# Performance work log

Hardware: AMD Instinct MI355X
Metric: run time of the kernel (lower is better)

The kernel has to match this reference:

```python
import jax, jax.numpy as jnp
import numpy as np

WIN_SIZE = 256           # GlobalConfig.win_size (assumed)
NFFT = 2 * WIN_SIZE      # 512 -> NFREQ = 257 rfft bins
HOP = WIN_SIZE
NFREQ = WIN_SIZE + 1
K = 3                    # all kernel sizes in the model
EPS = 1e-5


def _stft(x):
    # x: (B, S) -> (B, T, F, 2) real view of complex STFT (hann window, no center)
    B, S = x.shape
    T = (S - NFFT) // HOP + 1
    n = jnp.arange(NFFT)
    win = 0.5 - 0.5 * jnp.cos(2.0 * jnp.pi * n / NFFT)
    idx = jnp.arange(T)[:, None] * HOP + n[None, :]
    frames = x[:, idx] * win                       # (B, T, NFFT)
    spec = jnp.fft.rfft(frames, axis=-1)           # (B, T, F) complex
    return jnp.stack([spec.real, spec.imag], axis=-1).astype(x.dtype)


def _td_layer(x, W, b, same):
    # time-distributed conv over the frequency axis. x: (B,T,F,Cin), W: (k,Cin,Cout)
    k = W.shape[0]
    if same:
        x = jnp.pad(x, ((0, 0), (0, 0), (k // 2, k - 1 - k // 2), (0, 0)))
    Fout = x.shape[2] - k + 1
    xs = jnp.stack([x[:, :, i:i + Fout] for i in range(k)], axis=0)  # (k,B,T,Fout,Cin)
    return jnp.einsum('kbtfc,kco->btfo', xs, W) + b


def _td_block(x, W1, b1, W2, b2):
    h = jax.nn.relu(_td_layer(x, W1, b1, True))
    return _td_layer(h, W2, b2, True)


def _layer(x, g, beta, dw, W1, b1, W2, b2):
    # LayerNorm over (F, C), causal depthwise conv over T, TD pointwise block, ReLU
    B, T, F, C = x.shape
    mu = x.mean(axis=(-2, -1), keepdims=True)
    var = x.var(axis=(-2, -1), keepdims=True)
    xn = (x - mu) * jax.lax.rsqrt(var + EPS) * g + beta
    h = xn.reshape(B, T, F * C)
    hp = jnp.pad(h, ((0, 0), (K - 1, 0), (0, 0)))   # causal left-pad on time
    y = sum(hp[:, i:i + T, :] * dw[:, i] for i in range(K))  # (B,T,F*C) depthwise
    y = y.reshape(B, T, F, C)
    return jax.nn.relu(_td_block(y, W1, b1, W2, b2))


def setup_inputs() -> dict:
    key = jax.random.key(0)
    ks = iter(jax.random.split(key, 40))
    def rn(shape, s=0.05):
        return (jax.random.normal(next(ks), shape) * s).astype(jnp.float32)
    F = NFREQ
    d = {}
    d['x'] = jax.random.normal(next(ks), (8, 262144), dtype=jnp.float32)
    d['l0_W1'] = rn((3, 2, 4)); d['l0_b1'] = jnp.zeros((4,), jnp.float32)
    d['l0_W2'] = rn((3, 4, 8)); d['l0_b2'] = jnp.zeros((8,), jnp.float32)
    for name, cin in (('l1', 8), ('l2', 16), ('l3', 24)):
        d[name + '_g'] = jnp.ones((F, cin), jnp.float32)
        d[name + '_bn'] = jnp.zeros((F, cin), jnp.float32)
        d[name + '_dw'] = rn((F * cin, 3), 0.3)
        d[name + '_W1'] = rn((3, cin, 8)); d[name + '_b1'] = jnp.zeros((8,), jnp.float32)
        d[name + '_W2'] = rn((3, 8, 8)); d[name + '_b2'] = jnp.zeros((8,), jnp.float32)
    d['fc1_W'] = rn((3, 32, 1)); d['fc1_b'] = jnp.zeros((1,), jnp.float32)
    d['fc2_W'] = rn((F - 2, 1)); d['fc2_b'] = jnp.zeros((1,), jnp.float32)
    return d


def reference(x, l0_W1, l0_b1, l0_W2, l0_b2,
              l1_g, l1_bn, l1_dw, l1_W1, l1_b1, l1_W2, l1_b2,
              l2_g, l2_bn, l2_dw, l2_W1, l2_b1, l2_W2, l2_b2,
              l3_g, l3_bn, l3_dw, l3_W1, l3_b1, l3_W2, l3_b2,
              fc1_W, fc1_b, fc2_W, fc2_b):
    s = _stft(x)                                            # (B,T,F,2)
    h = jax.nn.relu(_td_block(s, l0_W1, l0_b1, l0_W2, l0_b2))  # (B,T,F,8)
    h = jnp.concatenate([h, _layer(h, l1_g, l1_bn, l1_dw, l1_W1, l1_b1, l1_W2, l1_b2)], axis=3)
    h = jnp.concatenate([h, _layer(h, l2_g, l2_bn, l2_dw, l2_W1, l2_b1, l2_W2, l2_b2)], axis=3)
    h = jnp.concatenate([h, _layer(h, l3_g, l3_bn, l3_dw, l3_W1, l3_b1, l3_W2, l3_b2)], axis=3)
    h = jax.nn.relu(_td_layer(h, fc1_W, fc1_b, False))[..., 0]  # (B,T,F-2)
    out = jax.nn.sigmoid(h @ fc2_W + fc2_b)                 # (B,T,1)
    return out[..., 0]                                      # (B,T)
```

## Files before the change

kernel.cpp:

```cpp
#include <hip/hip_runtime.h>
#include <hip/hip_fp16.h>

namespace {

constexpr int BATCH = 8;
constexpr int SLEN  = 262144;
constexpr int TT    = 1023;
constexpr int NF    = 257;
constexpr int NCH   = 24;
constexpr int NBT   = BATCH * TT;
constexpr int FRS   = NCH * NF;
constexpr float EPS = 1e-5f;

typedef _Float16 h2v __attribute__((ext_vector_type(2)));

__device__ inline float fdot2(unsigned a, unsigned b, float c) {
#if __has_builtin(__builtin_amdgcn_fdot2)
  return __builtin_amdgcn_fdot2(__builtin_bit_cast(h2v, a),
                                __builtin_bit_cast(h2v, b), c, false);
#else
  h2v av = __builtin_bit_cast(h2v, a), bv = __builtin_bit_cast(h2v, b);
  return fmaf((float)av[0], (float)bv[0], fmaf((float)av[1], (float)bv[1], c));
#endif
}
__device__ inline unsigned packh2(float a, float b) {
  h2v v; v[0] = (_Float16)a; v[1] = (_Float16)b;
  return __builtin_bit_cast(unsigned, v);
}
__device__ inline unsigned short f2h(float v) {
  return __builtin_bit_cast(unsigned short, (_Float16)v);
}
__device__ inline int div257(int e) { return (e * 65282) >> 24; }

__global__ __launch_bounds__(256, 8) void stft_l0_kernel(
    const float* __restrict__ x,
    const float* __restrict__ W1g, const float* __restrict__ b1g,
    const float* __restrict__ W2g, const float* __restrict__ b2g,
    __half* __restrict__ H, float* __restrict__ stats0)
{
  __shared__ float  xw[512];
  __shared__ __align__(16) float2 abE[128];
  __shared__ __align__(16) float2 abO[128];
  __shared__ float2 oxc[128];
  __shared__ float  sre[NF + 2];
  __shared__ float  sim[NF + 2];
  __shared__ float  h1[4][NF + 2];
  __shared__ float  wW1[24], wb1[4], wW2[96], wb2[8];
  __shared__ float  red[8];

  const int tid = threadIdx.x;
  const int bt  = blockIdx.x;
  const int b   = bt / TT;
  const int t   = bt - b * TT;
  const float* xp = x + (size_t)b * SLEN + (size_t)t * 256;

  if (tid < 24) wW1[tid] = W1g[tid];
  if (tid < 4)  wb1[tid] = b1g[tid];
  if (tid < 96) wW2[tid] = W2g[tid];
  if (tid < 8)  wb2[tid] = b2g[tid];

  const float STEP = 6.283185307179586f / 512.0f;
  for (int n = tid; n < 512; n += 256) {
    float sv, cv;
    sincosf(STEP * (float)n, &sv, &cv);
    xw[n] = xp[n] * (0.5f - 0.5f * cv);
  }
  __syncthreads();

  if (tid < 128) {
    const int n = 2 * tid;
    abE[tid] = (n == 0) ? make_float2(0.f, 0.f)
                        : make_float2(xw[n] + xw[512 - n], xw[n] - xw[512 - n]);
  } else {
    const int n = 2 * (tid - 128) + 1;
    abO[tid - 128] = make_float2(xw[n] + xw[512 - n], xw[n] - xw[512 - n]);
  }
  __syncthreads();

  const float x0 = xw[0], x256 = xw[256];
  {
    const int  k = tid & 127;
    const bool P = (tid >= 128);
    float s1, c1;
    sincosf(STEP * (float)k, &s1, &c1);
    const float c2 = fmaf(c1,c1,-s1*s1), s2 = 2.f*c1*s1;
    const float c3 = fmaf(c2,c1,-s2*s1), s3 = fmaf(c2,s1, s2*c1);
    const float c4 = fmaf(c2,c2,-s2*s2), s4 = 2.f*c2*s2;
    const float c5 = fmaf(c4,c1,-s4*s1), s5 = fmaf(c4,s1, s4*c1);
    const float c6 = fmaf(c4,c2,-s4*s2), s6 = fmaf(c4,s2, s4*c2);
    const float c7 = fmaf(c4,c3,-s4*s3), s7 = fmaf(c4,s3, s4*c3);
    const float c8 = fmaf(c4,c4,-s4*s4), s8 = 2.f*c4*s4;
    float cA = P ? c1 : 1.f, sA = P ? s1 : 0.f;
    float cB = P ? c3 : c2,  sB = P ? s3 : s2;
    float cC = P ? c5 : c4,  sC = P ? s5 : s4;
    float cD = P ? c7 : c6,  sD = P ? s7 : s6;
    const float4* ab4 = P ? (const float4*)abO : (const float4*)abE;
    float re = 0.f, im = 0.f;
    for (int m = 0; m < 32; ++m) {
      const float4 q0 = ab4[2*m];
      const float4 q1 = ab4[2*m + 1];
      re = fmaf(q0.x, cA, re); im = fmaf(q0.y, sA, im);
      re = fmaf(q0.z, cB, re); im = fmaf(q0.w, sB, im);
      re = fmaf(q1.x, cC, re); im = fmaf(q1.y, sC, im);
      re = fmaf(q1.z, cD, re); im = fmaf(q1.w, sD, im);
      float t0;
      t0 = fmaf(cA, c8, -sA*s8); sA = fmaf(cA, s8, sA*c8); cA = t0;
      t0 = fmaf(cB, c8, -sB*s8); sB = fmaf(cB, s8, sB*c8); cB = t0;
      t0 = fmaf(cC, c8, -sC*s8); sC = fmaf(cC, s8, sC*c8); cC = t0;
      t0 = fmaf(cD, c8, -sD*s8); sD = fmaf(cD, s8, sD*c8); cD = t0;
    }
    if (P) oxc[k] = make_float2(re, im);

    float tr = 0.f, ti = 0.f;
    if (tid & 1) {
      const float v = abO[tid >> 1].y;
      ti = ((tid >> 1) & 1) ? v : -v;
    } else {
      const float v = abE[tid >> 1].x;
      tr = ((tid >> 1) & 1) ? -v : v;
    }
    #pragma unroll
    for (int off = 32; off > 0; off >>= 1) {
      tr += __shfl_down(tr, off, 64);
      ti += __shfl_down(ti, off, 64);
    }
    if ((tid & 63) == 0) { red[(tid >> 6)*2] = tr; red[(tid >> 6)*2 + 1] = ti; }
    __syncthreads();

    if (!P) {
      const float rb  = x0 + ((k & 1) ? -x256 : x256);
      const float reo = oxc[k].x, imo = oxc[k].y;
      sre[1 + k]       = rb + re + reo;
      sim[1 + k]       = -(im + imo);
      sre[1 + 256 - k] = rb + re - reo;
      sim[1 + 256 - k] = im - imo;
    }
    if (tid == 0) {
      sre[1 + 128] = x0 + x256 + red[0] + red[2] + red[4] + red[6];
      sim[1 + 128] = red[1] + red[3] + red[5] + red[7];
      sre[0] = 0.f; sim[0] = 0.f; sre[258] = 0.f; sim[258] = 0.f;
    }
  }
  __syncthreads();

  for (int f = tid; f < NF; f += 256) {
    float acc[4] = {wb1[0], wb1[1], wb1[2], wb1[3]};
    #pragma unroll
    for (int i = 0; i < 3; ++i) {
      float vr = sre[f + i], vi = sim[f + i];
      #pragma unroll
      for (int c = 0; c < 4; ++c)
        acc[c] = fmaf(vr, wW1[(i*2+0)*4 + c], fmaf(vi, wW1[(i*2+1)*4 + c], acc[c]));
    }
    #pragma unroll
    for (int c = 0; c < 4; ++c) h1[c][f + 1] = fmaxf(acc[c], 0.f);
  }
  if (tid < 4) { h1[tid][0] = 0.f; h1[tid][NF + 1] = 0.f; }
  __syncthreads();

  const size_t obase = (size_t)bt * FRS;
  float ps1 = 0.f, ps2 = 0.f;
  for (int f = tid; f < NF; f += 256) {
    float acc[8];
    #pragma unroll
    for (int c = 0; c < 8; ++c) acc[c] = wb2[c];
    #pragma unroll
    for (int i = 0; i < 3; ++i)
      #pragma unroll
      for (int c4 = 0; c4 < 4; ++c4) {
        float hv = h1[c4][f + i];
        #pragma unroll
        for (int c = 0; c < 8; ++c)
          acc[c] = fmaf(hv, wW2[(i*4+c4)*8 + c], acc[c]);
      }
    #pragma unroll
    for (int c = 0; c < 8; ++c) {
      const __half hv = __float2half(fmaxf(acc[c], 0.f));
      H[obase + (size_t)c * NF + f] = hv;
      const float v = __half2float(hv);
      ps1 += v;
      ps2 = fmaf(v, v, ps2);
    }
  }
  #pragma unroll
  for (int off = 32; off > 0; off >>= 1) {
    ps1 += __shfl_down(ps1, off, 64);
    ps2 += __shfl_down(ps2, off, 64);
  }
  __syncthreads();
  if ((tid & 63) == 0) { red[(tid >> 6) * 2] = ps1; red[(tid >> 6) * 2 + 1] = ps2; }
  __syncthreads();
  if (tid == 0) {
    stats0[bt * 2]     = red[0] + red[2] + red[4] + red[6];
    stats0[bt * 2 + 1] = red[1] + red[3] + red[5] + red[7];
  }
}

__device__ inline void fold_one(int idx, int CIN,
    const float* g, const float* bn, const float* dw, __half* dst, int NEL) {
  const int c = div257(idx), f = idx - c * 257;
  const int s = f * CIN + c;
  const float gv = g[s], bv = bn[s];
  const float d0 = dw[s*3], d1 = dw[s*3+1], d2 = dw[s*3+2];
  dst[idx]         = __float2half(gv * d0);
  dst[NEL + idx]   = __float2half(gv * d1);
  dst[2*NEL + idx] = __float2half(gv * d2);
  dst[3*NEL + idx] = __float2half(bv * (d0 + d1 + d2));
  dst[4*NEL + idx] = __float2half(bv * (d1 + d2));
  dst[5*NEL + idx] = __float2half(bv * d2);
}

__global__ __launch_bounds__(256) void fold_all(
    const float* g1, const float* bn1, const float* dw1, __half* t1,
    const float* g2, const float* bn2, const float* dw2, __half* t2,
    const float* g3, const float* bn3, const float* dw3, __half* t3)
{
  int idx = blockIdx.x * 256 + threadIdx.x;
  if (idx < 8*257) { fold_one(idx, 8, g1, bn1, dw1, t1, 8*257); return; }
  idx -= 8*257;
  if (idx < 16*257) { fold_one(idx, 16, g2, bn2, dw2, t2, 16*257); return; }
  idx -= 16*257;
  if (idx < 24*257) fold_one(idx, 24, g3, bn3, dw3, t3, 24*257);
}

template<int CIN, bool HEAD>
__global__ __launch_bounds__(256, 8) void layer_bt(
    const __half* __restrict__ H, __half* __restrict__ Hout,
    const float* __restrict__ st0, const float* __restrict__ st1,
    const float* __restrict__ st2, float* __restrict__ stats_out,
    const __half* __restrict__ tbl,
    const float* __restrict__ W1g, const float* __restrict__ b1g,
    const float* __restrict__ W2g, const float* __restrict__ b2g,
    const float* __restrict__ fc1W, const float* __restrict__ fc1b,
    const float* __restrict__ fc2W, const float* __restrict__ fc2b,
    float* __restrict__ out)
{
  constexpr int NEL   = CIN * NF;
  constexpr int NP2   = NEL / 2;
  constexpr int NPER2 = (NP2 + 255) / 256;
  constexpr int TAIL2 = NP2 - 256 * (NPER2 - 1);
  constexpr int PC1   = CIN + 2;
  constexpr int PC2   = 10;
  constexpr int NQ1   = CIN / 2;

  __shared__ unsigned short y_t[259 * PC1];
  __shared__ unsigned short h1_t[259 * PC2];
  __shared__ unsigned w1p[3 * NQ1 * 8];
  __shared__ unsigned w2p[96];
  __shared__ float wb1[8], wb2[8];
  __shared__ float red[8];
  __shared__ unsigned wfc1p[HEAD ? 48 : 1];

  const int tid = threadIdx.x;
  const int bt  = blockIdx.x;
  const int b   = bt / TT;
  const int t   = bt - b * TT;

  for (int idx = tid; idx < 3 * NQ1 * 8; idx += 256) {
    const int o = idx & 7, q = (idx >> 3) % NQ1, i = idx / (NQ1 * 8);
    w1p[idx] = packh2(W1g[(i*CIN + 2*q)*8 + o], W1g[(i*CIN + 2*q + 1)*8 + o]);
  }
  if (tid < 96) {
    const int o = tid & 7, q = (tid >> 3) & 3, i = tid >> 5;
    w2p[tid] = packh2(W2g[(i*8 + 2*q)*8 + o], W2g[(i*8 + 2*q + 1)*8 + o]);
  }
  if (tid < 8) { wb1[tid] = b1g[tid]; wb2[tid] = b2g[tid]; }
  if (tid < PC1) { y_t[tid] = 0; y_t[258*PC1 + tid] = 0; }
  if (tid < PC2) { h1_t[tid] = 0; h1_t[258*PC2 + tid] = 0; }
  if constexpr (HEAD) {
    if (tid < 48) {
      const int q = tid & 15, i = tid >> 4;
      wfc1p[tid] = packh2(fc1W[i*32 + 2*q], fc1W[i*32 + 2*q + 1]);
    }
  }

  float mu0 = 0.f, rs0 = 0.f, mu1 = 0.f, rs1 = 0.f, mu2, rs2;
  {
    const float inv = 1.0f / (float)NEL;
    float s1 = st0[bt*2], s2v = st0[bt*2+1];
    if constexpr (CIN >= 16) { s1 += st1[bt*2]; s2v += st1[bt*2+1]; }
    if constexpr (CIN >= 24) { s1 += st2[bt*2]; s2v += st2[bt*2+1]; }
    mu2 = s1 * inv; rs2 = rsqrtf(s2v * inv - mu2*mu2 + EPS);
    if (t >= 1) {
      const int fb = bt - 1;
      float a = st0[fb*2], c = st0[fb*2+1];
      if constexpr (CIN >= 16) { a += st1[fb*2]; c += st1[fb*2+1]; }
      if constexpr (CIN >= 24) { a += st2[fb*2]; c += st2[fb*2+1]; }
      mu1 = a * inv; rs1 = rsqrtf(c * inv - mu1*mu1 + EPS);
    }
    if (t >= 2) {
      const int fb = bt - 2;
      float a = st0[fb*2], c = st0[fb*2+1];
      if constexpr (CIN >= 16) { a += st1[fb*2]; c += st1[fb*2+1]; }
      if constexpr (CIN >= 24) { a += st2[fb*2]; c += st2[fb*2+1]; }
      mu0 = a * inv; rs0 = rsqrtf(c * inv - mu0*mu0 + EPS);
    }
  }

  const int base = b * TT;
  const __half2* f2p = (const __half2*)(H + (size_t)bt * FRS);
  const __half2* f1p = (const __half2*)(H + (size_t)max(bt - 1, base) * FRS);
  const __half2* f0p = (const __half2*)(H + (size_t)max(bt - 2, base) * FRS);
  const __half2* P0p = (const __half2*)tbl;
  const __half2* P1p = (const __half2*)(tbl + NEL);
  const __half2* P2p = (const __half2*)(tbl + 2 * NEL);
  const int qsel = (t >= 2) ? 0 : (t == 1 ? 1 : 2);
  const __half2* Qp  = (const __half2*)(tbl + (3 + qsel) * NEL);

  #pragma unroll
  for (int j = 0; j < NPER2; ++j) {
    const bool act = (j < NPER2 - 1) || (tid < TAIL2);
    if (act) {
      const int p  = tid + 256 * j;
      const int e0 = 2 * p;
      const int c0 = div257(e0);
      const int fi = e0 - c0 * 257;
      const float2 xa = __half22float2(f0p[p]);
      const float2 xb = __half22float2(f1p[p]);
      const float2 xc = __half22float2(f2p[p]);
      const float2 pa = __half22float2(P0p[p]);
      const float2 pb = __half22float2(P1p[p]);
      const float2 pc = __half22float2(P2p[p]);
      const float2 qq = __half22float2(Qp[p]);
      const float y0 = fmaf((xa.x - mu0) * rs0, pa.x,
                       fmaf((xb.x - mu1) * rs1, pb.x,
                       fmaf((xc.x - mu2) * rs2, pc.x, qq.x)));
      const float y1 = fmaf((xa.y - mu0) * rs0, pa.y,
                       fmaf((xb.y - mu1) * rs1, pb.y,
                       fmaf((xc.y - mu2) * rs2, pc.y, qq.y)));
      const int a1 = (fi + 1) * PC1 + c0;
      y_t[a1] = f2h(y0);
      const int a2 = (fi == 256) ? (PC1 + c0 + 1) : (a1 + PC1);
      y_t[a2] = f2h(y1);
    }
  }
  __syncthreads();

  {
    const int f = tid;
    float acc[8];
    #pragma unroll
    for (int c = 0; c < 8; ++c) acc[c] = wb1[c];
    const unsigned* yw = (const unsigned*)y_t;
    #pragma unroll
    for (int i = 0; i < 3; ++i) {
      const unsigned* row = yw + (f + i) * (PC1 / 2);
      for (int q = 0; q < NQ1; ++q) {
        const unsigned yv = row[q];
        #pragma unroll
        for (int c = 0; c < 8; ++c)
          acc[c] = fdot2(yv, w1p[(i * NQ1 + q) * 8 + c], acc[c]);
      }
    }
    unsigned* hw = (unsigned*)h1_t + (f + 1) * (PC2 / 2);
    #pragma unroll
    for (int k = 0; k < 4; ++k)
      hw[k] = packh2(fmaxf(acc[2*k], 0.f), fmaxf(acc[2*k+1], 0.f));
  }
  if (tid < 8) {
    float a = wb1[tid];
    const unsigned* yw = (const unsigned*)y_t;
    #pragma unroll
    for (int i = 0; i < 3; ++i) {
      const unsigned* row = yw + (256 + i) * (PC1 / 2);
      for (int q = 0; q < NQ1; ++q)
        a = fdot2(row[q], w1p[(i * NQ1 + q) * 8 + tid], a);
    }
    h1_t[257 * PC2 + tid] = f2h(fmaxf(a, 0.f));
  }
  __syncthreads();

  float ps1 = 0.f, ps2 = 0.f;
  {
    const int f = tid;
    float o2[8];
    #pragma unroll
    for (int c = 0; c < 8; ++c) o2[c] = wb2[c];
    const unsigned* hw = (const unsigned*)h1_t;
    #pragma unroll
    for (int i = 0; i < 3; ++i) {
      const unsigned* row = hw + (f + i) * (PC2 / 2);
      #pragma unroll
      for (int q = 0; q < 4; ++q) {
        const unsigned hv = row[q];
        #pragma unroll
        for (int c = 0; c < 8; ++c)
          o2[c] = fdot2(hv, w2p[(i*4 + q)*8 + c], o2[c]);
      }
    }
    if constexpr (!HEAD) {
      const size_t ob = (size_t)bt * FRS + (size_t)CIN * NF;
      #pragma unroll
      for (int c = 0; c < 8; ++c) {
        const __half hv = __float2half(fmaxf(o2[c], 0.f));
        Hout[ob + (size_t)c * NF + f] = hv;
        const float v = __half2float(hv);
        ps1 += v;
        ps2 = fmaf(v, v, ps2);
      }
    } else {
      unsigned* ow = (unsigned*)y_t + f * (PC1 / 2);
      #pragma unroll
      for (int k = 0; k < 4; ++k)
        ow[k] = packh2(fmaxf(o2[2*k], 0.f), fmaxf(o2[2*k+1], 0.f));
    }
  }
  if (tid >= 8 && tid < 16) {
    const int c8 = tid - 8;
    float a = wb2[c8];
    const unsigned* hw = (const unsigned*)h1_t;
    #pragma unroll
    for (int i = 0; i < 3; ++i) {
      const unsigned* row = hw + (256 + i) * (PC2 / 2);
      #pragma unroll
      for (int q = 0; q < 4; ++q)
        a = fdot2(row[q], w2p[(i*4 + q)*8 + c8], a);
    }
    if constexpr (!HEAD) {
      const size_t ob = (size_t)bt * FRS + (size_t)CIN * NF;
      const __half hv = __float2half(fmaxf(a, 0.f));
      Hout[ob + (size_t)c8 * NF + 256] = hv;
      const float v = __half2float(hv);
      ps1 += v;
      ps2 = fmaf(v, v, ps2);
    } else {
      y_t[256 * PC1 + c8] = f2h(fmaxf(a, 0.f));
    }
  }

  if constexpr (!HEAD) {
    #pragma unroll
    for (int off = 32; off > 0; off >>= 1) {
      ps1 += __shfl_down(ps1, off, 64);
      ps2 += __shfl_down(ps2, off, 64);
    }
    if ((tid & 63) == 0) { red[(tid >> 6)*2] = ps1; red[(tid >> 6)*2+1] = ps2; }
    __syncthreads();
    if (tid == 0) {
      stats_out[bt*2]     = red[0] + red[2] + red[4] + red[6];
      stats_out[bt*2 + 1] = red[1] + red[3] + red[5] + red[7];
    }
  } else {
    __syncthreads();
    float part = 0.f;
    if (tid < NF - 2) {
      const unsigned short* xgu = (const unsigned short*)f2p;
      float acc = fc1b[0];
      #pragma unroll
      for (int i = 0; i < 3; ++i) {
        const int pos = tid + i;
        for (int q = 0; q < 12; ++q) {
          const unsigned lo = xgu[(2*q) * 257 + pos];
          const unsigned hi = xgu[(2*q + 1) * 257 + pos];
          acc = fdot2(lo | (hi << 16), wfc1p[i*16 + q], acc);
        }
        const unsigned* orow = (const unsigned*)y_t + pos * (PC1 / 2);
        #pragma unroll
        for (int q = 0; q < 4; ++q)
          acc = fdot2(orow[q], wfc1p[i*16 + 12 + q], acc);
      }
      part = fmaxf(acc, 0.f) * fc2W[tid];
    }
    #pragma unroll
    for (int off = 32; off > 0; off >>= 1) part += __shfl_down(part, off, 64);
    if ((tid & 63) == 0) red[tid >> 6] = part;
    __syncthreads();
    if (tid == 0) {
      const float tot = red[0] + red[1] + red[2] + red[3] + fc2b[0];
      out[bt] = 1.0f / (1.0f + expf(-tot));
    }
  }
}

}

extern "C" void kernel_launch(void* const* d_in, const int* in_sizes, int n_in,
                              void* d_out, int out_size, void* d_ws, size_t ws_size,
                              hipStream_t stream) {
  (void)in_sizes; (void)n_in; (void)out_size; (void)ws_size;
  const float* x = (const float*)d_in[0];
  float* out = (float*)d_out;
  char*  wsb = (char*)d_ws;

  __half* H   = (__half*)wsb;
  char* p = wsb + (size_t)NBT * FRS * sizeof(__half);
  float* st0  = (float*)p; p += 2 * NBT * sizeof(float);
  float* st1  = (float*)p; p += 2 * NBT * sizeof(float);
  float* st2  = (float*)p; p += 2 * NBT * sizeof(float);
  __half* tbl1 = (__half*)p; p += 6 * (8  * NF) * sizeof(__half);
  __half* tbl2 = (__half*)p; p += 6 * (16 * NF) * sizeof(__half);
  __half* tbl3 = (__half*)p;

  dim3 blk(256);

  fold_all<<<dim3((48 * 257 + 255) / 256), blk, 0, stream>>>(
      (const float*)d_in[5],  (const float*)d_in[6],  (const float*)d_in[7],  tbl1,
      (const float*)d_in[12], (const float*)d_in[13], (const float*)d_in[14], tbl2,
      (const float*)d_in[19], (const float*)d_in[20], (const float*)d_in[21], tbl3);

  stft_l0_kernel<<<dim3(NBT), blk, 0, stream>>>(
      x, (const float*)d_in[1], (const float*)d_in[2],
      (const float*)d_in[3], (const float*)d_in[4], H, st0);

  layer_bt<8, false><<<dim3(NBT), blk, 0, stream>>>(
      H, H, st0, nullptr, nullptr, st1, tbl1,
      (const float*)d_in[8], (const float*)d_in[9],
      (const float*)d_in[10], (const float*)d_in[11],
      nullptr, nullptr, nullptr, nullptr, nullptr);

  layer_bt<16, false><<<dim3(NBT), blk, 0, stream>>>(
      H, H, st0, st1, nullptr, st2, tbl2,
      (const float*)d_in[15], (const float*)d_in[16],
      (const float*)d_in[17], (const float*)d_in[18],
      nullptr, nullptr, nullptr, nullptr, nullptr);

  layer_bt<24, true><<<dim3(NBT), blk, 0, stream>>>(
      H, nullptr, st0, st1, st2, nullptr, tbl3,
      (const float*)d_in[22], (const float*)d_in[23],
      (const float*)d_in[24], (const float*)d_in[25],
      (const float*)d_in[26], (const float*)d_in[27],
      (const float*)d_in[28], (const float*)d_in[29],
      out);
}
```

Baseline: 431.4 us.

## Vectorize layer input loads to uint4, use half2 math, stage head input in LDS

The LayerNorm and depthwise-conv prologue now loads eight fp16 values per thread with 128-bit loads instead of two. It computes the normalized causal conv in packed half2 FMAs with the rsqrt and mean folded in. The head variant also transposes the current frame into a new LDS buffer, so the fc1 dot products read packed rows instead of strided global halfwords, and its launch-bounds occupancy hint drops to 4. This aims to cut global load instructions and uncoalesced reads. In exchange it adds fp16 accumulation error, more LDS use and a scalar fallback path for groups that cross a channel boundary.

```diff
diff --git a/kernel.cpp b/kernel.cpp
--- a/kernel.cpp
+++ b/kernel.cpp
@@ -30,6 +30,7 @@
 __device__ inline unsigned short f2h(float v) {
   return __builtin_bit_cast(unsigned short, (_Float16)v);
 }
+__device__ inline __half2 u2h(unsigned u) { return __builtin_bit_cast(__half2, u); }
 __device__ inline int div257(int e) { return (e * 65282) >> 24; }
 
 __global__ __launch_bounds__(256, 8) void stft_l0_kernel(
@@ -224,7 +225,7 @@
 }
 
 template<int CIN, bool HEAD>
-__global__ __launch_bounds__(256, 8) void layer_bt(
+__global__ __launch_bounds__(256, HEAD ? 4 : 8) void layer_bt(
     const __half* __restrict__ H, __half* __restrict__ Hout,
     const float* __restrict__ st0, const float* __restrict__ st1,
     const float* __restrict__ st2, float* __restrict__ stats_out,
@@ -235,16 +236,16 @@
     const float* __restrict__ fc2W, const float* __restrict__ fc2b,
     float* __restrict__ out)
 {
-  constexpr int NEL   = CIN * NF;
-  constexpr int NP2   = NEL / 2;
-  constexpr int NPER2 = (NP2 + 255) / 256;
-  constexpr int TAIL2 = NP2 - 256 * (NPER2 - 1);
-  constexpr int PC1   = CIN + 2;
-  constexpr int PC2   = 10;
-  constexpr int NQ1   = CIN / 2;
+  constexpr int NEL  = CIN * NF;
+  constexpr int NU4  = NEL / 8;
+  constexpr int NJ4  = (NU4 + 255) / 256;
+  constexpr int PC1  = CIN + 2;
+  constexpr int PC2  = 10;
+  constexpr int NQ1  = CIN / 2;
 
   __shared__ unsigned short y_t[259 * PC1];
   __shared__ unsigned short h1_t[259 * PC2];
+  __shared__ unsigned short x_t[HEAD ? 257 * 26 : 1];
   __shared__ unsigned w1p[3 * NQ1 * 8];
   __shared__ unsigned w2p[96];
   __shared__ float wb1[8], wb2[8];
@@ -296,42 +297,88 @@
       mu0 = a * inv; rs0 = rsqrtf(c * inv - mu0*mu0 + EPS);
     }
   }
+  const __half2 rs0h = __float2half2_rn(rs0);
+  const __half2 rs1h = __float2half2_rn(rs1);
+  const __half2 rs2h = __float2half2_rn(rs2);
+  const __half2 nm0h = __float2half2_rn(-mu0);
+  const __half2 nm1h = __float2half2_rn(-mu1);
+  const __half2 nm2h = __float2half2_rn(-mu2);
 
   const int base = b * TT;
-  const __half2* f2p = (const __half2*)(H + (size_t)bt * FRS);
-  const __half2* f1p = (const __half2*)(H + (size_t)max(bt - 1, base) * FRS);
-  const __half2* f0p = (const __half2*)(H + (size_t)max(bt - 2, base) * FRS);
-  const __half2* P0p = (const __half2*)tbl;
-  const __half2* P1p = (const __half2*)(tbl + NEL);
-  const __half2* P2p = (const __half2*)(tbl + 2 * NEL);
+  const uint4* F2 = (const uint4*)(H + (size_t)bt * FRS);
+  const uint4* F1 = (const uint4*)(H + (size_t)max(bt - 1, base) * FRS);
+  const uint4* F0 = (const uint4*)(H + (size_t)max(bt - 2, base) * FRS);
+  const uint4* P0 = (const uint4*)tbl;
+  const uint4* P1 = (const uint4*)(tbl + NEL);
+  const uint4* P2 = (const uint4*)(tbl + 2 * NEL);
   const int qsel = (t >= 2) ? 0 : (t == 1 ? 1 : 2);
-  const __half2* Qp  = (const __half2*)(tbl + (3 + qsel) * NEL);
+  const uint4* Qq = (const uint4*)(tbl + (3 + qsel) * NEL);
 
   #pragma unroll
-  for (int j = 0; j < NPER2; ++j) {
-    const bool act = (j < NPER2 - 1) || (tid < TAIL2);
-    if (act) {
-      const int p  = tid + 256 * j;
-      const int e0 = 2 * p;
+  for (int j = 0; j < NJ4; ++j) {
+    const int v = tid + 256 * j;
+    if (v < NU4) {
+      const uint4 X0 = F0[v], X1 = F1[v], X2 = F2[v];
+      const uint4 A = P0[v], B = P1[v], C = P2[v], Qw = Qq[v];
+      unsigned r[4], xr[4];
+      const unsigned aw[4] = {A.x, A.y, A.z, A.w};
+      const unsigned bw[4] = {B.x, B.y, B.z, B.w};
+      const unsigned cw[4] = {C.x, C.y, C.z, C.w};
+      const unsigned qw[4] = {Qw.x, Qw.y, Qw.z, Qw.w};
+      const unsigned x0w[4] = {X0.x, X0.y, X0.z, X0.w};
+      const unsigned x1w[4] = {X1.x, X1.y, X1.z, X1.w};
+      const unsigned x2w[4] = {X2.x, X2.y, X2.z, X2.w};
+      #pragma unroll
+      for (int w = 0; w < 4; ++w) {
+        const __half2 rp0 = __hmul2(rs0h, u2h(aw[w]));
+        const __half2 rp1 = __hmul2(rs1h, u2h(bw[w]));
+        const __half2 rp2 = __hmul2(rs2h, u2h(cw[w]));
+        __half2 acc = __hfma2(nm0h, rp0, u2h(qw[w]));
+        acc = __hfma2(nm1h, rp1, acc);
+        acc = __hfma2(nm2h, rp2, acc);
+        acc = __hfma2(u2h(x0w[w]), rp0, acc);
+        acc = __hfma2(u2h(x1w[w]), rp1, acc);
+        acc = __hfma2(u2h(x2w[w]), rp2, acc);
+        r[w]  = __builtin_bit_cast(unsigned, acc);
+        xr[w] = x2w[w];
+      }
+      const int e0 = 8 * v;
       const int c0 = div257(e0);
-      const int fi = e0 - c0 * 257;
-      const float2 xa = __half22float2(f0p[p]);
-      const float2 xb = __half22float2(f1p[p]);
-      const float2 xc = __half22float2(f2p[p]);
-      const float2 pa = __half22float2(P0p[p]);
-      const float2 pb = __half22float2(P1p[p]);
-      const float2 pc = __half22float2(P2p[p]);
-      const float2 qq = __half22float2(Qp[p]);
-      const float y0 = fmaf((xa.x - mu0) * rs0, pa.x,
-                       fmaf((xb.x - mu1) * rs1, pb.x,
-                       fmaf((xc.x - mu2) * rs2, pc.x, qq.x)));
-      const float y1 = fmaf((xa.y - mu0) * rs0, pa.y,
-                       fmaf((xb.y - mu1) * rs1, pb.y,
-                       fmaf((xc.y - mu2) * rs2, pc.y, qq.y)));
-      const int a1 = (fi + 1) * PC1 + c0;
-      y_t[a1] = f2h(y0);
-      const int a2 = (fi == 256) ? (PC1 + c0 + 1) : (a1 + PC1);
-      y_t[a2] = f2h(y1);
+      const int fi = e0 - 257 * c0;
+      if (fi <= 249) {
+        int a = (fi + 1) * PC1 + c0;
+        #pragma unroll
+        for (int w = 0; w < 4; ++w) {
+          y_t[a]       = (unsigned short)(r[w] & 0xffffu);
+          y_t[a + PC1] = (unsigned short)(r[w] >> 16);
+          a += 2 * PC1;
+        }
+        if constexpr (HEAD) {
+          int xa = fi * 26 + c0;
+          #pragma unroll
+          for (int w = 0; w < 4; ++w) {
+            x_t[xa]      = (unsigned short)(xr[w] & 0xffffu);
+            x_t[xa + 26] = (unsigned short)(xr[w] >> 16);
+            xa += 52;
+          }
+        }
+      } else {
+        #pragma unroll
+        for (int w = 0; w < 4; ++w) {
+          #pragma unroll
+          for (int h = 0; h < 2; ++h) {
+            const int e = e0 + 2 * w + h;
+            const int c = div257(e);
+            const int f = e - 257 * c;
+            const unsigned short val =
+                (unsigned short)(h ? (r[w] >> 16) : (r[w] & 0xffffu));
+            y_t[(f + 1) * PC1 + c] = val;
+            if constexpr (HEAD)
+              x_t[f * 26 + c] =
+                  (unsigned short)(h ? (xr[w] >> 16) : (xr[w] & 0xffffu));
+          }
+        }
+      }
     }
   }
   __syncthreads();
@@ -444,16 +491,13 @@
     __syncthreads();
     float part = 0.f;
     if (tid < NF - 2) {
-      const unsigned short* xgu = (const unsigned short*)f2p;
       float acc = fc1b[0];
       #pragma unroll
       for (int i = 0; i < 3; ++i) {
         const int pos = tid + i;
-        for (int q = 0; q < 12; ++q) {
-          const unsigned lo = xgu[(2*q) * 257 + pos];
-          const unsigned hi = xgu[(2*q + 1) * 257 + pos];
-          acc = fdot2(lo | (hi << 16), wfc1p[i*16 + q], acc);
-        }
+        const unsigned* xrow = (const unsigned*)x_t + pos * 13;
+        for (int q = 0; q < 12; ++q)
+          acc = fdot2(xrow[q], wfc1p[i*16 + q], acc);
         const unsigned* orow = (const unsigned*)y_t + pos * (PC1 / 2);
         #pragma unroll
         for (int q = 0; q < 4; ++q)
```

Result: slower. 447.8 us (+3.8%).
